# Kernel tuning notes

Measured on AMD Instinct MI355X. Metric: run time of the kernel, lower is better.

Reference implementation:

```python
import jax, jax.numpy as jnp
import numpy as np

K = 3  # kernel_size; padding = 1, stride = 1


def setup_inputs() -> dict:
    key = jax.random.key(0)
    ks = jax.random.split(key, 3)
    b, c, h, w = 8, 96, 256, 256
    x = jax.random.normal(ks[0], (b, c, h, w), dtype=jnp.float32)
    # attention MLP params: 1x1 convs on pooled vector == dense layers
    w1 = jax.random.normal(ks[1], (c // 8, c), dtype=jnp.float32) * (1.0 / np.sqrt(c))
    b1 = jnp.zeros((c // 8,), dtype=jnp.float32)
    w2 = jax.random.normal(ks[2], (K * K, c // 8), dtype=jnp.float32) * (1.0 / np.sqrt(c // 8))
    b2 = jnp.zeros((K * K,), dtype=jnp.float32)
    return {"x": x, "w1": w1, "b1": b1, "w2": w2, "b2": b2}


def reference(x, w1, b1, w2, b2):
    b, c, h, w = x.shape
    # attention: global avg pool -> 1x1 conv -> relu -> 1x1 conv -> softmax over k^2
    pooled = x.mean(axis=(2, 3))                       # (b, c)
    hid = jax.nn.relu(pooled @ w1.T + b1)              # (b, c//8)
    kw = jax.nn.softmax(hid @ w2.T + b2, axis=1)       # (b, k^2), per-batch kernel
    # dynamic depthwise conv: weighted sum of k^2 shifted views (no unfold materialization)
    xp = jnp.pad(x, ((0, 0), (0, 0), (1, 1), (1, 1)))
    out = jnp.zeros_like(x)
    for p in range(K * K):  # F.unfold ordering: row-major over kernel window
        di, dj = p // K, p % K
        out = out + kw[:, p, None, None, None] * xp[:, :, di:di + h, dj:dj + w]
    return out
```

## Files before the change

### kernel.cpp

```cpp
#include <hip/hip_runtime.h>
#include <math.h>


#define NB 8
#define NC 96
#define HH 256
#define WW 256
#define PLANE (HH * WW)
#define NPLANES (NB * NC)

typedef float vfloat4 __attribute__((ext_vector_type(4)));

__global__ __launch_bounds__(256) void pool_kernel(const float* __restrict__ x,
                                                   float* __restrict__ pooled) {
    const int plane = blockIdx.x;
    const int tid = threadIdx.x;
    const vfloat4* xp = (const vfloat4*)x + (size_t)plane * (PLANE / 4);
    float s = 0.f;
#pragma unroll 8
    for (int k = 0; k < 64; ++k) {
        vfloat4 v = xp[k * 256 + tid];
        s += v.x + v.y + v.z + v.w;
    }
#pragma unroll
    for (int off = 32; off > 0; off >>= 1) s += __shfl_down(s, off);
    __shared__ float ws[4];
    if ((tid & 63) == 0) ws[tid >> 6] = s;
    __syncthreads();
    if (tid == 0)
        pooled[plane] = (ws[0] + ws[1] + ws[2] + ws[3]) * (1.0f / (float)PLANE);
}

__global__ __launch_bounds__(128) void attn_kernel(const float* __restrict__ pooled,
                                                   const float* __restrict__ w1,
                                                   const float* __restrict__ b1,
                                                   const float* __restrict__ w2,
                                                   const float* __restrict__ b2,
                                                   float* __restrict__ kw) {
    const int b = blockIdx.x;
    const int tid = threadIdx.x;
    __shared__ float p[NC];
    __shared__ float hid[12];
    __shared__ float logit[9];
    if (tid < NC) p[tid] = pooled[b * NC + tid];
    __syncthreads();
    if (tid < 12) {
        float a = b1[tid];
#pragma unroll
        for (int c = 0; c < NC; ++c) a = fmaf(p[c], w1[tid * NC + c], a);
        hid[tid] = a > 0.f ? a : 0.f;
    }
    __syncthreads();
    if (tid < 9) {
        float a = b2[tid];
#pragma unroll
        for (int j = 0; j < 12; ++j) a = fmaf(hid[j], w2[tid * 12 + j], a);
        logit[tid] = a;
    }
    __syncthreads();
    if (tid == 0) {
        float m = logit[0];
#pragma unroll
        for (int q = 1; q < 9; ++q) m = fmaxf(m, logit[q]);
        float e[9], s = 0.f;
#pragma unroll
        for (int q = 0; q < 9; ++q) { e[q] = __expf(logit[q] - m); s += e[q]; }
        float inv = 1.f / s;
#pragma unroll
        for (int q = 0; q < 9; ++q) kw[b * 9 + q] = e[q] * inv;
    }
}

struct Row {
    vfloat4 v;
    float hl, hr;
};

__device__ __forceinline__ Row load_row(const float* __restrict__ rowp, int lane) {
    Row r;
    r.v = *(const vfloat4*)(rowp + (lane << 2));
    float up = __shfl_up(r.v.w, 1);
    float dn = __shfl_down(r.v.x, 1);
    r.hl = (lane == 0) ? 0.f : up;
    r.hr = (lane == 63) ? 0.f : dn;
    return r;
}

__device__ __forceinline__ Row zero_row() {
    Row r; r.v = (vfloat4){0.f, 0.f, 0.f, 0.f}; r.hl = 0.f; r.hr = 0.f; return r;
}

__device__ __forceinline__ void row_fma(const Row& r, float wl, float wc, float wr,
                                        vfloat4& o) {
    o.x = fmaf(wl, r.hl,  fmaf(wc, r.v.x, fmaf(wr, r.v.y, o.x)));
    o.y = fmaf(wl, r.v.x, fmaf(wc, r.v.y, fmaf(wr, r.v.z, o.y)));
    o.z = fmaf(wl, r.v.y, fmaf(wc, r.v.z, fmaf(wr, r.v.w, o.z)));
    o.w = fmaf(wl, r.v.z, fmaf(wc, r.v.w, fmaf(wr, r.hr,  o.w)));
}

__global__ __launch_bounds__(256) void conv_kernel(const float* __restrict__ x,
                                                   const float* __restrict__ kw9,
                                                   float* __restrict__ out) {
    const int lane = threadIdx.x & 63;
    const int strip = (blockIdx.x << 2) + (threadIdx.x >> 6);
    const int rs = strip << 5;

    const size_t base = ((size_t)(blockIdx.z * NC + blockIdx.y)) * PLANE;
    const float* xpl = x + base;
    float* opl = out + base;

    float w[9];
#pragma unroll
    for (int p = 0; p < 9; ++p) w[p] = kw9[blockIdx.z * 9 + p];

    Row a = (rs == 0) ? zero_row() : load_row(xpl + (size_t)(rs - 1) * WW, lane);
    Row b = load_row(xpl + (size_t)rs * WW, lane);

#pragma unroll 4
    for (int i = rs; i < rs + 32; ++i) {
        Row c = (i + 1 < HH) ? load_row(xpl + (size_t)(i + 1) * WW, lane)
                             : zero_row();
        vfloat4 o = (vfloat4){0.f, 0.f, 0.f, 0.f};
        row_fma(a, w[0], w[1], w[2], o);
        row_fma(b, w[3], w[4], w[5], o);
        row_fma(c, w[6], w[7], w[8], o);
        __builtin_nontemporal_store(o, (vfloat4*)(opl + (size_t)i * WW + (lane << 2)));
        a = b; b = c;
    }
}

extern "C" void kernel_launch(void* const* d_in, const int* in_sizes, int n_in,
                              void* d_out, int out_size, void* d_ws, size_t ws_size,
                              hipStream_t stream) {
    const float* x  = (const float*)d_in[0];
    const float* w1 = (const float*)d_in[1];
    const float* b1 = (const float*)d_in[2];
    const float* w2 = (const float*)d_in[3];
    const float* b2 = (const float*)d_in[4];
    float* out = (float*)d_out;

    float* pooled = (float*)d_ws;
    float* kw     = pooled + NPLANES;

    pool_kernel<<<NPLANES, 256, 0, stream>>>(x, pooled);
    attn_kernel<<<NB, 128, 0, stream>>>(pooled, w1, b1, w2, b2, kw);
    dim3 grid(2, NC, NB);
    conv_kernel<<<grid, 256, 0, stream>>>(x, kw, out);
}
```

Baseline: 374.1 us.

## Split pooling into partial blocks, halve conv strips, prefetch next row

The pooling kernel now launches four blocks per plane that each write a partial sum, and the attention kernel combines the partials and applies the mean scaling. The conv kernel processes 16-row strips instead of 32, which doubles the grid, and it software-prefetches the row two ahead of the current output row. The goal is more parallelism and better latency hiding on a memory-bound workload. The cost is more blocks, a little extra halo reloading per strip and some extra register pressure.

```diff
diff --git a/kernel.cpp b/kernel.cpp
--- a/kernel.cpp
+++ b/kernel.cpp
@@ -12,26 +12,26 @@
 typedef float vfloat4 __attribute__((ext_vector_type(4)));
 
 __global__ __launch_bounds__(256) void pool_kernel(const float* __restrict__ x,
-                                                   float* __restrict__ pooled) {
-    const int plane = blockIdx.x;
+                                                   float* __restrict__ partial) {
+    const int blk = blockIdx.x;
     const int tid = threadIdx.x;
-    const vfloat4* xp = (const vfloat4*)x + (size_t)plane * (PLANE / 4);
+    const vfloat4* xp = (const vfloat4*)x + (size_t)(blk >> 2) * (PLANE / 4)
+                        + (size_t)(blk & 3) * 4096;
     float s = 0.f;
-#pragma unroll 8
-    for (int k = 0; k < 64; ++k) {
+#pragma unroll
+    for (int k = 0; k < 16; ++k) {
         vfloat4 v = xp[k * 256 + tid];
-        s += v.x + v.y + v.z + v.w;
+        s += (v.x + v.y) + (v.z + v.w);
     }
 #pragma unroll
     for (int off = 32; off > 0; off >>= 1) s += __shfl_down(s, off);
     __shared__ float ws[4];
     if ((tid & 63) == 0) ws[tid >> 6] = s;
     __syncthreads();
-    if (tid == 0)
-        pooled[plane] = (ws[0] + ws[1] + ws[2] + ws[3]) * (1.0f / (float)PLANE);
+    if (tid == 0) partial[blk] = (ws[0] + ws[1]) + (ws[2] + ws[3]);
 }
 
-__global__ __launch_bounds__(128) void attn_kernel(const float* __restrict__ pooled,
+__global__ __launch_bounds__(128) void attn_kernel(const float* __restrict__ partial,
                                                    const float* __restrict__ w1,
                                                    const float* __restrict__ b1,
                                                    const float* __restrict__ w2,
@@ -42,7 +42,10 @@
     __shared__ float p[NC];
     __shared__ float hid[12];
     __shared__ float logit[9];
-    if (tid < NC) p[tid] = pooled[b * NC + tid];
+    if (tid < NC) {
+        const float* pp = partial + ((size_t)(b * NC + tid) << 2);
+        p[tid] = ((pp[0] + pp[1]) + (pp[2] + pp[3])) * (1.0f / (float)PLANE);
+    }
     __syncthreads();
     if (tid < 12) {
         float a = b1[tid];
@@ -76,18 +79,21 @@
     float hl, hr;
 };
 
-__device__ __forceinline__ Row load_row(const float* __restrict__ rowp, int lane) {
+__device__ __forceinline__ vfloat4 raw_row(const float* __restrict__ xpl, int r,
+                                           int lane) {
+    if ((unsigned)r < (unsigned)HH)
+        return *(const vfloat4*)(xpl + (size_t)r * WW + (lane << 2));
+    return (vfloat4){0.f, 0.f, 0.f, 0.f};
+}
+
+__device__ __forceinline__ Row make_row(vfloat4 v, int lane) {
     Row r;
-    r.v = *(const vfloat4*)(rowp + (lane << 2));
-    float up = __shfl_up(r.v.w, 1);
-    float dn = __shfl_down(r.v.x, 1);
+    r.v = v;
+    float up = __shfl_up(v.w, 1);
+    float dn = __shfl_down(v.x, 1);
     r.hl = (lane == 0) ? 0.f : up;
     r.hr = (lane == 63) ? 0.f : dn;
     return r;
-}
-
-__device__ __forceinline__ Row zero_row() {
-    Row r; r.v = (vfloat4){0.f, 0.f, 0.f, 0.f}; r.hl = 0.f; r.hr = 0.f; return r;
 }
 
 __device__ __forceinline__ void row_fma(const Row& r, float wl, float wc, float wr,
@@ -103,7 +109,7 @@
                                                    float* __restrict__ out) {
     const int lane = threadIdx.x & 63;
     const int strip = (blockIdx.x << 2) + (threadIdx.x >> 6);
-    const int rs = strip << 5;
+    const int rs = strip << 4;
 
     const size_t base = ((size_t)(blockIdx.z * NC + blockIdx.y)) * PLANE;
     const float* xpl = x + base;
@@ -113,19 +119,21 @@
 #pragma unroll
     for (int p = 0; p < 9; ++p) w[p] = kw9[blockIdx.z * 9 + p];
 
-    Row a = (rs == 0) ? zero_row() : load_row(xpl + (size_t)(rs - 1) * WW, lane);
-    Row b = load_row(xpl + (size_t)rs * WW, lane);
+    Row a = make_row(raw_row(xpl, rs - 1, lane), lane);
+    Row b = make_row(raw_row(xpl, rs, lane), lane);
+    vfloat4 pre = raw_row(xpl, rs + 1, lane);
 
 #pragma unroll 4
-    for (int i = rs; i < rs + 32; ++i) {
-        Row c = (i + 1 < HH) ? load_row(xpl + (size_t)(i + 1) * WW, lane)
-                             : zero_row();
+    for (int i = rs; i < rs + 16; ++i) {
+        vfloat4 nxt = (i + 2 <= rs + 16) ? raw_row(xpl, i + 2, lane)
+                                         : (vfloat4){0.f, 0.f, 0.f, 0.f};
+        Row c = make_row(pre, lane);
         vfloat4 o = (vfloat4){0.f, 0.f, 0.f, 0.f};
         row_fma(a, w[0], w[1], w[2], o);
         row_fma(b, w[3], w[4], w[5], o);
         row_fma(c, w[6], w[7], w[8], o);
         __builtin_nontemporal_store(o, (vfloat4*)(opl + (size_t)i * WW + (lane << 2)));
-        a = b; b = c;
+        a = b; b = c; pre = nxt;
     }
 }
 
@@ -139,11 +147,11 @@
     const float* b2 = (const float*)d_in[4];
     float* out = (float*)d_out;
 
-    float* pooled = (float*)d_ws;
-    float* kw     = pooled + NPLANES;
+    float* partial = (float*)d_ws;
+    float* kw      = partial + NPLANES * 4;
 
-    pool_kernel<<<NPLANES, 256, 0, stream>>>(x, pooled);
-    attn_kernel<<<NB, 128, 0, stream>>>(pooled, w1, b1, w2, b2, kw);
-    dim3 grid(2, NC, NB);
+    pool_kernel<<<NPLANES * 4, 256, 0, stream>>>(x, partial);
+    attn_kernel<<<NB, 128, 0, stream>>>(partial, w1, b1, w2, b2, kw);
+    dim3 grid(4, NC, NB);
     conv_kernel<<<grid, 256, 0, stream>>>(x, kw, out);
 }
```

New measurement: 379.0 us. About the same (+1.3%).
